# Performance work log

Hardware: AMD Instinct MI355X
Metric: run time of the kernel (lower is better)

Reference implementation:

```python
import math
import jax, jax.numpy as jnp
import numpy as np

B, T, D, V, S, R = 128, 32, 64, 4096, 32, 8
PONDER = 0.01
TWO_PI = np.float32(2.0 * math.pi)


def _ln(x, g, b, eps=1e-5):
    mu = x.mean(-1, keepdims=True)
    var = ((x - mu) ** 2).mean(-1, keepdims=True)
    return (x - mu) / jnp.sqrt(var + eps) * g + b


def _clin(xr, xi, Wr, br, Wi, bi):
    # ComplexLinear: fc_real/fc_imag share biases per torch module
    real = (xr @ Wr + br) - (xi @ Wi + bi)
    imag = (xi @ Wr + br) + (xr @ Wi + bi)
    return real, imag


def setup_inputs() -> dict:
    key = jax.random.key(0)
    ks = jax.random.split(key, 10)
    f = lambda k, sh, s: jax.random.normal(k, sh, jnp.float32) * s
    return {
        "x_seq": jax.random.randint(ks[0], (B, T), 0, V),
        "enc_emb": f(ks[1], (V, 2 * D), 0.02),
        "vq_emb": f(ks[2], (V, 2 * D), 0.05),
        "norm_rg": jnp.ones((D,), jnp.float32),
        "norm_rb": jnp.zeros((D,), jnp.float32),
        "norm_ig": jnp.ones((D,), jnp.float32),
        "norm_ib": jnp.zeros((D,), jnp.float32),
        "proj_w": f(ks[3], (3, 2, D, D), 0.05),  # [q/k/v, real/imag, in, out]
        "proj_b": f(ks[4], (3, 2, D), 0.01),
        "mem_gate_w": f(ks[5], (2 * D, 1), 0.05),
        "mem_gate_b": jnp.zeros((1,), jnp.float32),
        "arb_w": f(ks[6], (2 * D, 3), 0.05),
        "arb_b": jnp.zeros((3,), jnp.float32),
        "dec_w": f(ks[7], (2 * D, V), 0.02),
        "dec_b": jnp.zeros((V,), jnp.float32),
        "halt_bias": jnp.array(3.0, jnp.float32),
        "input_gate": jnp.array(0.0, jnp.float32),
    }


def _fwd(x_seq, enc_emb, vq_emb, norm_rg, norm_rb, norm_ig, norm_ib,
         proj_w, proj_b, mem_gate_w, mem_gate_b, arb_w, arb_b,
         dec_w, dec_b, halt_bias, input_gate):
    sg = jax.lax.stop_gradient
    emb = enc_emb[x_seq]                         # [B,T,2D]
    er, ei = emb[..., :D], emb[..., D:]
    alpha = jax.nn.sigmoid(input_gate)
    bias = jax.nn.softplus(halt_bias)
    vq_sq = (vq_emb ** 2).sum(-1)                # [V]

    def step(carry, xs):
        gw_r, gw_i, mem_r, mem_i = carry
        x_r, x_i = xs
        gw_r = alpha * gw_r + (1.0 - alpha) * x_r
        gw_i = alpha * gw_i + (1.0 - alpha) * x_i
        active = jnp.ones((x_r.shape[0],), jnp.float32)
        acc_vq = jnp.zeros_like(active)
        acc_ppx = jnp.zeros_like(active)
        acc_ent = jnp.zeros_like(active)
        acc_pond = jnp.zeros_like(active)
        acc_ph = jnp.zeros_like(active)
        prev_ang = jnp.arctan2(gw_i, gw_r)
        for _ in range(R):
            cr = _ln(gw_r, norm_rg, norm_rb)
            ci = _ln(gw_i, norm_ig, norm_ib)
            flat = jnp.concatenate([cr, ci], -1)            # [B,2D]
            # VQ (argmin over squared euclidean == argmin over cdist)
            d2 = (flat ** 2).sum(-1, keepdims=True) - 2.0 * (flat @ vq_emb.T) + vq_sq
            idx = jnp.argmin(d2, -1)                        # [B]
            zq = vq_emb[idx]                                # [B,2D]
            vq_loss = ((zq - sg(flat)) ** 2).mean(-1) + 0.25 * ((sg(zq) - flat) ** 2).mean(-1)
            zq_st = flat + sg(zq - flat)                    # straight-through
            avg = jax.nn.one_hot(idx, V, dtype=jnp.float32).mean(0)
            ent = -(avg * jnp.log(avg + 1e-10)).sum()
            ppx = jnp.exp(ent)
            vq_r, vq_i = zq_st[:, :D], zq_st[:, D:]
            # Hermitian gating
            qr, qi = _clin(cr, ci, proj_w[0, 0], proj_b[0, 0], proj_w[0, 1], proj_b[0, 1])
            kr, ki = _clin(cr, ci, proj_w[1, 0], proj_b[1, 0], proj_w[1, 1], proj_b[1, 1])
            wr, wi = _clin(cr, ci, proj_w[2, 0], proj_b[2, 0], proj_w[2, 1], proj_b[2, 1])
            gate = jax.nn.sigmoid((qr * kr + qi * ki).sum(-1, keepdims=True))
            g_r, g_i = wr * gate, wi * gate
            # memory read (mem unchanged during recursion)
            sim = jnp.einsum('bsd,bd->bs', mem_r, cr) + jnp.einsum('bsd,bd->bs', mem_i, ci)
            attn = jax.nn.softmax(sim, -1)
            m_r = jnp.einsum('bs,bsd->bd', attn, mem_r)
            m_i = jnp.einsum('bs,bsd->bd', attn, mem_i)
            # arbitrator mix
            gates = jax.nn.softmax(flat @ arb_w + arb_b, -1)  # [B,3]
            u_r = gates[:, 0:1] * g_r + gates[:, 1:2] * m_r + gates[:, 2:3] * vq_r
            u_i = gates[:, 0:1] * g_i + gates[:, 1:2] * m_i + gates[:, 2:3] * vq_i
            c_r = 0.6 * cr + 0.4 * u_r
            c_i = 0.6 * ci + 0.4 * u_i
            ang = jnp.arctan2(c_i, c_r)
            diff = jnp.abs(ang - prev_ang)
            diff = jnp.minimum(diff, TWO_PI - diff)
            acc_ph = acc_ph + active * diff.mean(-1)
            prev_ang = ang
            halt = jax.nn.sigmoid(bias - vq_loss)
            stop = (halt > 0.5).astype(jnp.float32)
            acc_pond = acc_pond + active * PONDER
            m = active > 0.5
            acc_vq = jnp.where(m, vq_loss, acc_vq)
            acc_ppx = jnp.where(m, ppx, acc_ppx)
            acc_ent = jnp.where(m, ent, acc_ent)
            gw_r = jnp.where(m[:, None], c_r, gw_r)
            gw_i = jnp.where(m[:, None], c_i, gw_i)
            active = active * (1.0 - stop)
        # final memory write (read output discarded, matching torch)
        flat_gw = jnp.concatenate([gw_r, gw_i], -1)
        wg = jax.nn.sigmoid(flat_gw @ mem_gate_w + mem_gate_b)  # [B,1]
        sh_r = jnp.roll(mem_r, 1, axis=1)
        sh_i = jnp.roll(mem_i, 1, axis=1)
        mem_r = sh_r.at[:, 0].set(wg * gw_r + (1.0 - wg) * sh_r[:, 0])
        mem_i = sh_i.at[:, 0].set(wg * gw_i + (1.0 - wg) * sh_i[:, 0])
        stats = jnp.stack([acc_vq.mean(), acc_ppx.mean(), acc_ent.mean(),
                           acc_pond.mean(), acc_ph.mean()])
        return (gw_r, gw_i, mem_r, mem_i), (gw_r, gw_i, stats)

    init = (jnp.zeros((B, D), jnp.float32), jnp.zeros((B, D), jnp.float32),
            jnp.zeros((B, S, D), jnp.float32), jnp.zeros((B, S, D), jnp.float32))
    xs = (jnp.moveaxis(er, 1, 0), jnp.moveaxis(ei, 1, 0))
    (gw_r, gw_i, mem_r, mem_i), (o_r, o_i, stats) = jax.lax.scan(step, init, xs)
    flat_out = jnp.concatenate([jnp.moveaxis(o_r, 0, 1), jnp.moveaxis(o_i, 0, 1)], -1)  # [B,T,2D]
    logits = flat_out @ dec_w + dec_b
    return logits, stats.mean(0), mem_r, mem_i


def reference(x_seq, enc_emb, vq_emb, norm_rg, norm_rb, norm_ig, norm_ib,
              proj_w, proj_b, mem_gate_w, mem_gate_b, arb_w, arb_b,
              dec_w, dec_b, halt_bias, input_gate):
    return _fwd(x_seq, enc_emb, vq_emb, norm_rg, norm_rb, norm_ig, norm_ib,
                proj_w, proj_b, mem_gate_w, mem_gate_b, arb_w, arb_b,
                dec_w, dec_b, halt_bias, input_gate)
```

## Files before the change

### kernel.cpp

```cpp
#include <hip/hip_runtime.h>
#include <math.h>

#define BB 128
#define TT 32
#define DDIM 64
#define VV 4096
#define SS 32
#define RR 8
#define NT 512
#define SMP 65

typedef unsigned short u16;
typedef unsigned int u32;
typedef _Float16 h2 __attribute__((ext_vector_type(2)));

__device__ __forceinline__ h2 bch(u32 u){ union { u32 u; h2 h; } v; v.u = u; return v.h; }

__device__ __forceinline__ float fdot2f(u32 a, u32 b, float acc){
#if __has_builtin(__builtin_amdgcn_fdot2)
  return __builtin_amdgcn_fdot2(bch(a), bch(b), acc, false);
#else
  h2 x = bch(a), y = bch(b);
  return acc + (float)x[0] * (float)y[0] + (float)x[1] * (float)y[1];
#endif
}

__device__ __forceinline__ u32 packh2(float a, float b){
  union { _Float16 h[2]; u32 u; } p;
  p.h[0] = (_Float16)a; p.h[1] = (_Float16)b;
  return p.u;
}

__device__ __forceinline__ void bar(){ __syncthreads(); }

__global__ __launch_bounds__(256) void k_pack(const float* __restrict__ vq, u32* __restrict__ vqT){
  int gid = blockIdx.x * 256 + threadIdx.x;
  int l   = gid & 63;
  int dc8 = (gid >> 6) & 15;
  int c0  = gid >> 10;
  int c   = (c0 << 6) + l;
  const float4* s4 = (const float4*)(vq + c * 128 + dc8 * 8);
  float4 lo = s4[0], hi = s4[1];
  uint4 o;
  o.x = packh2(lo.x, lo.y);
  o.y = packh2(lo.z, lo.w);
  o.z = packh2(hi.x, hi.y);
  o.w = packh2(hi.z, hi.w);
  ((uint4*)vqT)[gid] = o;
}

__global__ __launch_bounds__(256) void k_vqsq(const float* __restrict__ vq, float* __restrict__ vqsq){
  int c = blockIdx.x * 256 + threadIdx.x;
  const float4* v4 = (const float4*)(vq + c * 128);
  float s = 0.f;
  #pragma unroll
  for (int d = 0; d < 32; d++){
    float4 v = v4[d];
    s = fmaf(v.x, v.x, s); s = fmaf(v.y, v.y, s);
    s = fmaf(v.z, v.z, s); s = fmaf(v.w, v.w, s);
  }
  vqsq[c] = s;
}

__global__ __launch_bounds__(NT) void k_recur(
    const int* __restrict__ x_seq, const float* __restrict__ enc_emb,
    const float* __restrict__ vq_emb, const u32* __restrict__ vqT,
    const float* __restrict__ vq_sq,
    const float* __restrict__ nrg, const float* __restrict__ nrb,
    const float* __restrict__ nig, const float* __restrict__ nib,
    const float* __restrict__ proj_w, const float* __restrict__ proj_b,
    const float* __restrict__ mgw, const float* __restrict__ mgb,
    const float* __restrict__ arb_w, const float* __restrict__ arb_b,
    const float* __restrict__ hb, const float* __restrict__ ig,
    float* __restrict__ gwout,
    int* __restrict__ idxbuf, int* __restrict__ rstop_g, float* __restrict__ accs,
    float* __restrict__ out_mem)
{
  const int b = blockIdx.x;
  const int tid = threadIdx.x;
  const int lane = tid & 63;
  const int wave = tid >> 6;

  __shared__ __align__(16) float s_gw[128];
  __shared__ __align__(16) float s_flat[128];
  __shared__ __align__(16) u32   s_flath[64];
  __shared__ __align__(16) float s_c[128];
  __shared__ __align__(16) float s_zq[128];
  __shared__ __align__(16) float s_enext[128];
  __shared__ float s_mem[2][SS][SMP];
  __shared__ __align__(16) float s_mv[12][DDIM];
  __shared__ float s_sim[SS];
  __shared__ float s_red[8];
  __shared__ float s_cand[8];
  __shared__ int   s_candi[8];

  for (int i = tid; i < 128; i += NT) s_gw[i] = 0.f;
  for (int i = tid; i < 2 * SS * SMP; i += NT) ((float*)s_mem)[i] = 0.f;
  if (tid < 128) s_enext[tid] = enc_emb[x_seq[b * TT] * 128 + tid];
  __syncthreads();

  const float alpha = 1.f / (1.f + expf(-ig[0]));
  float bias_h; { float x = hb[0]; bias_h = log1pf(expf(x)); }
  int head = 0;
  float prev_ang = 0.f;
  float acc_ph = 0.f;

  const float pb0r = proj_b[lane],        pb0i = proj_b[64 + lane];
  const float pb1r = proj_b[128 + lane],  pb1i = proj_b[192 + lane];
  const float pb2r = proj_b[256 + lane],  pb2i = proj_b[320 + lane];

  const uint4* vqT4 = (const uint4*)vqT;

  #pragma unroll 1
  for (int t = 0; t < TT; t++){
    if (tid < 128){
      s_gw[tid] = alpha * s_gw[tid] + (1.f - alpha) * s_enext[tid];
    }
    bar();
    if (wave == 2) prev_ang = atan2f(s_gw[64 + lane], s_gw[lane]);

    float vl_last = 0.f;
    if (wave == 2) acc_ph = 0.f;
    int rst = 0;
    bool stop = false;

    #pragma unroll 1
    for (int r = 0; r < RR; r++){
      if (wave < 2){
        float x = s_gw[wave * 64 + lane];
        float mu = x;
        #pragma unroll
        for (int m = 1; m < 64; m <<= 1) mu += __shfl_xor(mu, m);
        mu *= (1.f / 64.f);
        float dxl = x - mu;
        float vv = dxl * dxl;
        #pragma unroll
        for (int m = 1; m < 64; m <<= 1) vv += __shfl_xor(vv, m);
        vv *= (1.f / 64.f);
        float rs = 1.f / sqrtf(vv + 1e-5f);
        const float* g  = wave ? nig : nrg;
        const float* bb = wave ? nib : nrb;
        float fv = dxl * rs * g[lane] + bb[lane];
        s_flat[wave * 64 + lane] = fv;
        float pv = __shfl_xor(fv, 1);
        if ((lane & 1) == 0)
          s_flath[(wave * 64 + lane) >> 1] = packh2(fv, pv);
      }
      bar();

      uint4 F[16];
      {
        const uint4* sfh4 = (const uint4*)s_flath;
        #pragma unroll
        for (int i = 0; i < 16; i++) F[i] = sfh4[i];
      }
      float bsc = 3.4e38f; int bidx = 0;
      #pragma unroll 1
      for (int k = 0; k < 8; k++){
        int c0 = wave + 8 * k;
        int c  = (c0 << 6) + lane;
        float qv = vq_sq[c];
        const uint4* vp = vqT4 + (c0 * 16) * 64 + lane;
        uint4 U[16];
        #pragma unroll
        for (int dc8 = 0; dc8 < 16; dc8++) U[dc8] = vp[dc8 * 64];
        float a0 = 0.f, a1 = 0.f, a2 = 0.f, a3 = 0.f;
        #pragma unroll
        for (int dc8 = 0; dc8 < 16; dc8 += 4){
          a0 = fdot2f(U[dc8+0].x, F[dc8+0].x, a0); a0 = fdot2f(U[dc8+0].y, F[dc8+0].y, a0);
          a0 = fdot2f(U[dc8+0].z, F[dc8+0].z, a0); a0 = fdot2f(U[dc8+0].w, F[dc8+0].w, a0);
          a1 = fdot2f(U[dc8+1].x, F[dc8+1].x, a1); a1 = fdot2f(U[dc8+1].y, F[dc8+1].y, a1);
          a1 = fdot2f(U[dc8+1].z, F[dc8+1].z, a1); a1 = fdot2f(U[dc8+1].w, F[dc8+1].w, a1);
          a2 = fdot2f(U[dc8+2].x, F[dc8+2].x, a2); a2 = fdot2f(U[dc8+2].y, F[dc8+2].y, a2);
          a2 = fdot2f(U[dc8+2].z, F[dc8+2].z, a2); a2 = fdot2f(U[dc8+2].w, F[dc8+2].w, a2);
          a3 = fdot2f(U[dc8+3].x, F[dc8+3].x, a3); a3 = fdot2f(U[dc8+3].y, F[dc8+3].y, a3);
          a3 = fdot2f(U[dc8+3].z, F[dc8+3].z, a3); a3 = fdot2f(U[dc8+3].w, F[dc8+3].w, a3);
        }
        float dot = (a0 + a1) + (a2 + a3);
        float sc = qv - 2.f * dot;
        if (sc < bsc || (sc == bsc && c < bidx)){ bsc = sc; bidx = c; }
      }
      #pragma unroll
      for (int m = 1; m < 64; m <<= 1){
        float os = __shfl_xor(bsc, m);
        int   oi = __shfl_xor(bidx, m);
        if (os < bsc || (os == bsc && oi < bidx)){ bsc = os; bidx = oi; }
      }
      if (lane == 0){ s_cand[wave] = bsc; s_candi[wave] = bidx; }
      bar();

      if (wave >= 2){
        if (wave == 3 && r == 0 && t + 1 < TT){
          int xn = x_seq[b * TT + t + 1];
          s_enext[lane]      = enc_emb[xn * 128 + lane];
          s_enext[64 + lane] = enc_emb[xn * 128 + 64 + lane];
        }
        const int w2 = wave - 2;
        const int p = w2 >> 1, wsel = w2 & 1;
        const float* W = proj_w + ((p * 2 + wsel) << 12);
        float a0=0.f,a1=0.f,a2=0.f,a3=0.f;
        float b0=0.f,b1=0.f,b2=0.f,b3=0.f;
        #pragma unroll
        for (int i = 0; i < 64; i += 4){
          float4 xr4 = *(const float4*)&s_flat[i];
          float4 xi4 = *(const float4*)&s_flat[64 + i];
          float w0 = W[(i + 0) * 64 + lane];
          float w1 = W[(i + 1) * 64 + lane];
          float w2v= W[(i + 2) * 64 + lane];
          float w3 = W[(i + 3) * 64 + lane];
          a0 = fmaf(xr4.x, w0, a0); a1 = fmaf(xr4.y, w1, a1);
          a2 = fmaf(xr4.z, w2v, a2); a3 = fmaf(xr4.w, w3, a3);
          b0 = fmaf(xi4.x, w0, b0); b1 = fmaf(xi4.y, w1, b1);
          b2 = fmaf(xi4.z, w2v, b2); b3 = fmaf(xi4.w, w3, b3);
        }
        s_mv[w2 * 2 + 0][lane] = (a0 + a1) + (a2 + a3);
        s_mv[w2 * 2 + 1][lane] = (b0 + b1) + (b2 + b3);
      } else if (wave == 0){
        const int s2 = lane & 31, h = lane >> 5;
        const float* mrow = &s_mem[h][s2][0];
        const float* fx = s_flat + h * 64;
        float a0=0.f,a1=0.f,a2=0.f,a3=0.f;
        #pragma unroll
        for (int d = 0; d < 64; d += 4){
          a0 = fmaf(mrow[d + 0], fx[d + 0], a0);
          a1 = fmaf(mrow[d + 1], fx[d + 1], a1);
          a2 = fmaf(mrow[d + 2], fx[d + 2], a2);
          a3 = fmaf(mrow[d + 3], fx[d + 3], a3);
        }
        float p = (a0 + a1) + (a2 + a3);
        p += __shfl_xor(p, 32);
        float mx = p;
        #pragma unroll
        for (int m = 1; m < 32; m <<= 1) mx = fmaxf(mx, __shfl_xor(mx, m));
        float e = expf(p - mx);
        float sm = e;
        #pragma unroll
        for (int m = 1; m < 32; m <<= 1) sm += __shfl_xor(sm, m);
        if (lane < 32) s_sim[lane] = e / sm;
      } else {
        float bs = s_cand[0]; int bi = s_candi[0];
        #pragma unroll
        for (int w = 1; w < 8; w++){
          float os = s_cand[w]; int oi = s_candi[w];
          if (os < bs || (os == bs && oi < bi)){ bs = os; bi = oi; }
        }
        int imin = __builtin_amdgcn_readfirstlane(bi);
        float f0 = s_flat[lane], f1 = s_flat[64 + lane];
        float p0 = fmaf(f0, arb_w[lane * 3 + 0], f1 * arb_w[(64 + lane) * 3 + 0]);
        float p1 = fmaf(f0, arb_w[lane * 3 + 1], f1 * arb_w[(64 + lane) * 3 + 1]);
        float p2 = fmaf(f0, arb_w[lane * 3 + 2], f1 * arb_w[(64 + lane) * 3 + 2]);
        float z0 = vq_emb[imin * 128 + lane];
        float z1 = vq_emb[imin * 128 + 64 + lane];
        s_zq[lane]      = z0;
        s_zq[64 + lane] = z1;
        float d0 = z0 - f0, d1 = z1 - f1;
        float sq = d0 * d0 + d1 * d1;
        #pragma unroll
        for (int m = 1; m < 64; m <<= 1){
          p0 += __shfl_xor(p0, m); p1 += __shfl_xor(p1, m);
          p2 += __shfl_xor(p2, m); sq += __shfl_xor(sq, m);
        }
        if (lane == 0){
          s_red[4] = p0 + arb_b[0];
          s_red[5] = p1 + arb_b[1];
          s_red[6] = p2 + arb_b[2];
          s_red[0] = 1.25f * sq * (1.f / 128.f);
          idxbuf[(b * TT + t) * RR + r] = imin;
        }
      }
      bar();

      float vl = s_red[0];
      stop = (bias_h - vl) > 0.f;
      vl_last = vl; rst = r;

      if (tid < 128){
        float qr = s_mv[0][lane] - s_mv[3][lane] + pb0r - pb0i;
        float qi = s_mv[1][lane] + s_mv[2][lane] + pb0r + pb0i;
        float kr = s_mv[4][lane] - s_mv[7][lane] + pb1r - pb1i;
        float ki = s_mv[5][lane] + s_mv[6][lane] + pb1r + pb1i;
        float g = fmaf(qr, kr, qi * ki);
        #pragma unroll
        for (int m = 1; m < 64; m <<= 1) g += __shfl_xor(g, m);
        float gate = 1.f / (1.f + expf(-g));
        const int h = wave, j = lane;
        float m_reg = 0.f;
        #pragma unroll 8
        for (int s2 = 0; s2 < 32; s2++)
          m_reg = fmaf(s_sim[s2], s_mem[h][s2][j], m_reg);
        float l0 = s_red[4], l1 = s_red[5], l2 = s_red[6];
        float mx = fmaxf(l0, fmaxf(l1, l2));
        float e0 = expf(l0 - mx), e1 = expf(l1 - mx), e2 = expf(l2 - mx);
        float inv = 1.f / (e0 + e1 + e2);
        float zq = s_zq[tid];
        float wv = h ? (s_mv[9][j] + s_mv[10][j] + pb2r + pb2i)
                     : (s_mv[8][j] - s_mv[11][j] + pb2r - pb2i);
        float u = (e0 * inv) * (gate * wv) + (e1 * inv) * m_reg + (e2 * inv) * zq;
        float cv = 0.6f * s_flat[tid] + 0.4f * u;
        s_c[tid]  = cv;
        s_gw[tid] = cv;
      }
      bar();

      if (wave == 2){
        float ang = atan2f(s_c[64 + lane], s_c[lane]);
        float df = fabsf(ang - prev_ang);
        df = fminf(df, 6.28318530717958647692f - df);
        prev_ang = ang;
        #pragma unroll
        for (int m = 1; m < 64; m <<= 1) df += __shfl_xor(df, m);
        acc_ph += df * (1.f / 64.f);
        if ((stop || r == RR - 1) && lane == 0)
          accs[(b * TT + t) * 4 + 2] = acc_ph;
      }
      if (stop) break;
    }

    float pond = 0.01f * (float)(rst + 1);
    if (tid < 128) gwout[(b * TT + t) * 128 + tid] = s_gw[tid];
    head = (head + SS - 1) & (SS - 1);
    if (wave < 2){
      float p = fmaf(s_c[lane], mgw[lane], s_c[64 + lane] * mgw[64 + lane]);
      #pragma unroll
      for (int m = 1; m < 64; m <<= 1) p += __shfl_xor(p, m);
      float wg = 1.f / (1.f + expf(-(p + mgb[0])));
      const int h = wave, d0 = lane;
      float old = s_mem[h][head][d0];
      s_mem[h][head][d0] = wg * s_c[h * 64 + d0] + (1.f - wg) * old;
    }
    if (tid == 0){
      int o = b * TT + t;
      rstop_g[o] = rst;
      accs[o * 4 + 0] = vl_last;
      accs[o * 4 + 1] = pond;
    }
  }

  bar();
  for (int i = tid; i < SS * DDIM; i += NT){
    int s2 = i >> 6, d0 = i & 63;
    int ph = (head + s2) & (SS - 1);
    out_mem[b * SS * DDIM + i] = s_mem[0][ph][d0];
    out_mem[BB * SS * DDIM + b * SS * DDIM + i] = s_mem[1][ph][d0];
  }
}

__global__ __launch_bounds__(256) void k_max(const int* __restrict__ rstop_g,
                                             int* __restrict__ maxr,
                                             float* __restrict__ out_stats){
  __shared__ int sm[8][TT];
  int tid = threadIdx.x;
  int t = tid & 31, q = tid >> 5;
  int mx = 0;
  for (int b = q * 16; b < q * 16 + 16; b++) mx = max(mx, rstop_g[b * TT + t]);
  sm[q][t] = mx;
  __syncthreads();
  if (tid < TT){
    int m = sm[0][tid];
    #pragma unroll
    for (int qq = 1; qq < 8; qq++) m = max(m, sm[qq][tid]);
    maxr[tid] = m;
  } else if (tid >= 64 && tid < 69){
    out_stats[tid - 64] = 0.f;
  }
}

__global__ __launch_bounds__(256) void k_tail(
    const u32* __restrict__ vqT, const float* __restrict__ vq_sq,
    const float* __restrict__ gwout, const int* __restrict__ rstop_g,
    const int* __restrict__ maxr, int* __restrict__ idxbuf,
    const float* __restrict__ nrg, const float* __restrict__ nrb,
    const float* __restrict__ nig, const float* __restrict__ nib)
{
  int o = blockIdx.x;
  int t = o & (TT - 1);
  int rs = rstop_g[o];
  if (rs >= maxr[t]) return;
  __shared__ __align__(16) u32 sfh[64];
  __shared__ float s_cand[4];
  __shared__ int   s_candi[4];
  int tid = threadIdx.x, lane = tid & 63, wave = tid >> 6;
  if (wave < 2){
    float x = gwout[o * 128 + wave * 64 + lane];
    float mu = x;
    #pragma unroll
    for (int m = 1; m < 64; m <<= 1) mu += __shfl_xor(mu, m);
    mu *= (1.f / 64.f);
    float dxl = x - mu;
    float vv = dxl * dxl;
    #pragma unroll
    for (int m = 1; m < 64; m <<= 1) vv += __shfl_xor(vv, m);
    vv *= (1.f / 64.f);
    float rsn = 1.f / sqrtf(vv + 1e-5f);
    const float* g  = wave ? nig : nrg;
    const float* bb = wave ? nib : nrb;
    float fv = dxl * rsn * g[lane] + bb[lane];
    float pv = __shfl_xor(fv, 1);
    if ((lane & 1) == 0) sfh[(wave * 64 + lane) >> 1] = packh2(fv, pv);
  }
  __syncthreads();
  uint4 F[16];
  {
    const uint4* sfh4 = (const uint4*)sfh;
    #pragma unroll
    for (int i = 0; i < 16; i++) F[i] = sfh4[i];
  }
  float bsc = 3.4e38f; int bidx = 0;
  #pragma unroll 1
  for (int k = 0; k < 16; k++){
    int c0 = wave + 4 * k;
    const uint4* vp = ((const uint4*)vqT) + (c0 * 16) * 64 + lane;
    uint4 U[16];
    #pragma unroll
    for (int dc8 = 0; dc8 < 16; dc8++) U[dc8] = vp[dc8 * 64];
    float dot = 0.f;
    #pragma unroll
    for (int dc8 = 0; dc8 < 16; dc8++){
      dot = fdot2f(U[dc8].x, F[dc8].x, dot);
      dot = fdot2f(U[dc8].y, F[dc8].y, dot);
      dot = fdot2f(U[dc8].z, F[dc8].z, dot);
      dot = fdot2f(U[dc8].w, F[dc8].w, dot);
    }
    int c = c0 * 64 + lane;
    float sc = vq_sq[c] - 2.f * dot;
    if (sc < bsc || (sc == bsc && c < bidx)){ bsc = sc; bidx = c; }
  }
  #pragma unroll
  for (int m = 1; m < 64; m <<= 1){
    float os = __shfl_xor(bsc, m);
    int   oi = __shfl_xor(bidx, m);
    if (os < bsc || (os == bsc && oi < bidx)){ bsc = os; bidx = oi; }
  }
  if (lane == 0){ s_cand[wave] = bsc; s_candi[wave] = bidx; }
  __syncthreads();
  if (tid == 0){
    float bs = s_cand[0]; int bi = s_candi[0];
    for (int w = 1; w < 4; w++){
      float os = s_cand[w]; int oi = s_candi[w];
      if (os < bs || (os == bs && oi < bi)){ bs = os; bi = oi; }
    }
    for (int r = rs + 1; r < RR; r++) idxbuf[o * RR + r] = bi;
  }
}

__global__ __launch_bounds__(512) void k_stats(
    const int* __restrict__ idxbuf, const int* __restrict__ rstop_g,
    const float* __restrict__ accs, const int* __restrict__ maxr,
    float* __restrict__ out_stats)
{
  __shared__ int   s_vals[8][128];
  __shared__ float s_ent2[RR];
  __shared__ float s_part[8][5];
  const int t = blockIdx.x;
  int tid = threadIdx.x, lane = tid & 63, wave = tid >> 6;
  int mr = maxr[t];
  int r = wave;
  if (r <= mr){
    int v1 = idxbuf[(lane * TT + t) * RR + r];
    int v2 = idxbuf[((64 + lane) * TT + t) * RR + r];
    s_vals[wave][lane]      = v1;
    s_vals[wave][64 + lane] = v2;
    int c1 = 0, c2 = 0;
    for (int j = 0; j < 128; j++){
      int v = s_vals[wave][j];
      c1 += (v == v1); c2 += (v == v2);
    }
    float contrib = -(logf((float)c1 * (1.f / 128.f) + 1e-10f)
                    + logf((float)c2 * (1.f / 128.f) + 1e-10f)) * (1.f / 128.f);
    #pragma unroll
    for (int m = 1; m < 64; m <<= 1) contrib += __shfl_xor(contrib, m);
    if (lane == 0) s_ent2[r] = contrib;
  }
  __syncthreads();

  float sv = 0.f, sp = 0.f, se = 0.f, sn = 0.f, sh = 0.f;
  if (tid < BB){
    int o = tid * TT + t;
    int rs = rstop_g[o];
    float ent = s_ent2[rs];
    se = ent;
    sp = expf(ent);
    sv = accs[o * 4 + 0];
    sn = accs[o * 4 + 1];
    sh = accs[o * 4 + 2];
  }
  #pragma unroll
  for (int m = 1; m < 64; m <<= 1){
    sv += __shfl_xor(sv, m); sp += __shfl_xor(sp, m); se += __shfl_xor(se, m);
    sn += __shfl_xor(sn, m); sh += __shfl_xor(sh, m);
  }
  if (lane == 0){
    s_part[wave][0] = sv; s_part[wave][1] = sp; s_part[wave][2] = se;
    s_part[wave][3] = sn; s_part[wave][4] = sh;
  }
  __syncthreads();
  if (tid == 0){
    float a[5] = {0.f, 0.f, 0.f, 0.f, 0.f};
    for (int w = 0; w < 8; w++)
      for (int j = 0; j < 5; j++) a[j] += s_part[w][j];
    const float inv = 1.f / (float)(BB * TT);
    for (int j = 0; j < 5; j++) atomicAdd(&out_stats[j], a[j] * inv);
  }
}

__global__ __launch_bounds__(256) void k_dec(
    const float* __restrict__ gwout, const float* __restrict__ dec_w,
    const float* __restrict__ dec_b, float* __restrict__ out)
{
  __shared__ float At[32][128];
  int tid = threadIdx.x;
  int row0 = blockIdx.y * 32;
  int col0 = blockIdx.x * 256;
  {
    const float4* src = (const float4*)(gwout + row0 * 128);
    float4* dst = (float4*)&At[0][0];
    for (int i = tid; i < 1024; i += 256) dst[i] = src[i];
  }
  __syncthreads();
  int v = col0 + tid;
  float acc[32];
  #pragma unroll
  for (int r2 = 0; r2 < 32; r2++) acc[r2] = 0.f;
  for (int k = 0; k < 128; k += 4){
    float w0 = dec_w[(k + 0) * 4096 + v];
    float w1 = dec_w[(k + 1) * 4096 + v];
    float w2 = dec_w[(k + 2) * 4096 + v];
    float w3 = dec_w[(k + 3) * 4096 + v];
    #pragma unroll
    for (int r2 = 0; r2 < 32; r2++){
      float4 a = *(const float4*)&At[r2][k];
      acc[r2] = fmaf(a.x, w0, fmaf(a.y, w1, fmaf(a.z, w2, fmaf(a.w, w3, acc[r2]))));
    }
  }
  float bv = dec_b[v];
  for (int r2 = 0; r2 < 32; r2++)
    out[(row0 + r2) * 4096 + v] = acc[r2] + bv;
}

extern "C" void kernel_launch(void* const* d_in, const int* in_sizes, int n_in,
                              void* d_out, int out_size, void* d_ws, size_t ws_size,
                              hipStream_t stream){
  const int*   x_seq   = (const int*)  d_in[0];
  const float* enc_emb = (const float*)d_in[1];
  const float* vq_emb  = (const float*)d_in[2];
  const float* nrg     = (const float*)d_in[3];
  const float* nrb     = (const float*)d_in[4];
  const float* nig     = (const float*)d_in[5];
  const float* nib     = (const float*)d_in[6];
  const float* proj_w  = (const float*)d_in[7];
  const float* proj_b  = (const float*)d_in[8];
  const float* mgw     = (const float*)d_in[9];
  const float* mgb     = (const float*)d_in[10];
  const float* arb_w   = (const float*)d_in[11];
  const float* arb_b   = (const float*)d_in[12];
  const float* dec_w   = (const float*)d_in[13];
  const float* dec_b   = (const float*)d_in[14];
  const float* hb      = (const float*)d_in[15];
  const float* ig      = (const float*)d_in[16];

  char* ws = (char*)d_ws;
  u32*   vqT    = (u32*)  (ws + 0);
  float* vqsq   = (float*)(ws + 2097152);
  float* gwout  = (float*)(ws + 2113536);
  int*   idxbuf = (int*)  (ws + 6307840);
  int*   rstop  = (int*)  (ws + 6438912);
  float* accs   = (float*)(ws + 6455296);
  int*   maxr   = (int*)  (ws + 6520832);

  float* out = (float*)d_out;
  float* out_stats = out + 16777216;
  float* out_mem   = out + 16777221;

  k_pack <<<dim3(256), dim3(256), 0, stream>>>(vq_emb, vqT);
  k_vqsq <<<dim3(16),  dim3(256), 0, stream>>>(vq_emb, vqsq);
  k_recur<<<dim3(BB),  dim3(NT),  0, stream>>>(
      x_seq, enc_emb, vq_emb, vqT, vqsq,
      nrg, nrb, nig, nib, proj_w, proj_b, mgw, mgb, arb_w, arb_b, hb, ig,
      gwout, idxbuf, rstop, accs, out_mem);
  k_dec  <<<dim3(16, 128), dim3(256), 0, stream>>>(gwout, dec_w, dec_b, out);
  k_max  <<<dim3(1),   dim3(256), 0, stream>>>(rstop, maxr, out_stats);
  k_tail <<<dim3(BB * TT), dim3(256), 0, stream>>>(vqT, vqsq, gwout, rstop, maxr, idxbuf,
                                                   nrg, nrb, nig, nib);
  k_stats<<<dim3(TT),  dim3(512), 0, stream>>>(idxbuf, rstop, accs, maxr, out_stats);
}
```

Before: 636.4 us.

## Double-buffer VQ codebook streaming through LDS via async global_load_lds

The nearest-codebook search now stages each wave's fp16 codebook slices into a per-wave double buffer in LDS using global_load_lds, with explicit vmcnt waits so the next chunk loads while the current one is dotted. The vq_sq norms are also prefetched into registers before the loop. The aim is to hide global memory latency inside the serial per-step search and to cut register pressure from the 16 uint4 loads. In exchange it adds 128 KB of LDS per block, which may limit occupancy or exceed the LDS budget, and it relies on hand-written waitcnt ordering being correct.

```diff
diff --git a/kernel.cpp b/kernel.cpp
--- a/kernel.cpp
+++ b/kernel.cpp
@@ -9,6 +9,12 @@
 #define RR 8
 #define NT 512
 #define SMP 65
+
+#if defined(__has_builtin)
+#if __has_builtin(__builtin_amdgcn_global_load_lds)
+#define HAS_GLLDS 1
+#endif
+#endif
 
 typedef unsigned short u16;
 typedef unsigned int u32;
@@ -60,6 +66,38 @@
     s = fmaf(v.z, v.z, s); s = fmaf(v.w, v.w, s);
   }
   vqsq[c] = s;
+}
+
+#if HAS_GLLDS
+__device__ __forceinline__ void stage8(const uint4* gsrc, uint4* lds){
+  #pragma unroll
+  for (int j = 0; j < 8; j++)
+    __builtin_amdgcn_global_load_lds(
+        (const __attribute__((address_space(1))) void*)(gsrc + j * 64),
+        (__attribute__((address_space(3))) void*)(lds + j * 64),
+        16, 0, 0);
+}
+#endif
+
+__device__ __forceinline__ void dotLds(const uint4* buf, const uint4 (&F)[16], int off, int lane,
+                                       float& a0, float& a1, float& a2, float& a3){
+  #pragma unroll
+  for (int j = 0; j < 8; j += 4){
+    uint4 u0 = buf[(j + 0) * 64 + lane];
+    uint4 u1 = buf[(j + 1) * 64 + lane];
+    uint4 u2 = buf[(j + 2) * 64 + lane];
+    uint4 u3 = buf[(j + 3) * 64 + lane];
+    uint4 f0 = F[off + j + 0], f1 = F[off + j + 1];
+    uint4 f2 = F[off + j + 2], f3 = F[off + j + 3];
+    a0 = fdot2f(u0.x, f0.x, a0); a0 = fdot2f(u0.y, f0.y, a0);
+    a0 = fdot2f(u0.z, f0.z, a0); a0 = fdot2f(u0.w, f0.w, a0);
+    a1 = fdot2f(u1.x, f1.x, a1); a1 = fdot2f(u1.y, f1.y, a1);
+    a1 = fdot2f(u1.z, f1.z, a1); a1 = fdot2f(u1.w, f1.w, a1);
+    a2 = fdot2f(u2.x, f2.x, a2); a2 = fdot2f(u2.y, f2.y, a2);
+    a2 = fdot2f(u2.z, f2.z, a2); a2 = fdot2f(u2.w, f2.w, a2);
+    a3 = fdot2f(u3.x, f3.x, a3); a3 = fdot2f(u3.y, f3.y, a3);
+    a3 = fdot2f(u3.z, f3.z, a3); a3 = fdot2f(u3.w, f3.w, a3);
+  }
 }
 
 __global__ __launch_bounds__(NT) void k_recur(
@@ -93,6 +131,9 @@
   __shared__ float s_red[8];
   __shared__ float s_cand[8];
   __shared__ int   s_candi[8];
+#if HAS_GLLDS
+  __shared__ __align__(16) uint4 s_vstg[8][2][8][64];
+#endif
 
   for (int i = tid; i < 128; i += NT) s_gw[i] = 0.f;
   for (int i = tid; i < 2 * SS * SMP; i += NT) ((float*)s_mem)[i] = 0.f;
@@ -148,45 +189,65 @@
       }
       bar();
 
-      uint4 F[16];
       {
-        const uint4* sfh4 = (const uint4*)s_flath;
-        #pragma unroll
-        for (int i = 0; i < 16; i++) F[i] = sfh4[i];
+        uint4 F[16];
+        {
+          const uint4* sfh4 = (const uint4*)s_flath;
+          #pragma unroll
+          for (int i = 0; i < 16; i++) F[i] = sfh4[i];
+        }
+        float Q[8];
+        #pragma unroll
+        for (int k = 0; k < 8; k++) Q[k] = vq_sq[((wave + 8 * k) << 6) + lane];
+
+        float bsc = 3.4e38f; int bidx = 0;
+#if HAS_GLLDS
+        uint4* stg0 = &s_vstg[wave][0][0][0];
+        uint4* stg1 = &s_vstg[wave][1][0][0];
+        const uint4* base0 = vqT4 + (wave * 16) * 64 + lane;
+        stage8(base0,          stg0);
+        stage8(base0 + 8 * 64, stg1);
+        #pragma unroll 1
+        for (int k = 0; k < 8; k++){
+          asm volatile("s_waitcnt vmcnt(8)" ::: "memory");
+          float a0 = 0.f, a1 = 0.f, a2 = 0.f, a3 = 0.f;
+          dotLds(stg0, F, 0, lane, a0, a1, a2, a3);
+          if (k < 7)
+            stage8(vqT4 + ((wave + 8 * (k + 1)) * 16) * 64 + lane, stg0);
+          if (k < 7) asm volatile("s_waitcnt vmcnt(8)" ::: "memory");
+          else       asm volatile("s_waitcnt vmcnt(0)" ::: "memory");
+          dotLds(stg1, F, 8, lane, a0, a1, a2, a3);
+          if (k < 7)
+            stage8(vqT4 + ((wave + 8 * (k + 1)) * 16 + 8) * 64 + lane, stg1);
+          float dot = (a0 + a1) + (a2 + a3);
+          int c = ((wave + 8 * k) << 6) + lane;
+          float sc = Q[k] - 2.f * dot;
+          if (sc < bsc || (sc == bsc && c < bidx)){ bsc = sc; bidx = c; }
+        }
+#else
+        #pragma unroll 1
+        for (int k = 0; k < 8; k++){
+          int c = ((wave + 8 * k) << 6) + lane;
+          const uint4* vp = vqT4 + ((wave + 8 * k) * 16) * 64 + lane;
+          uint4 U[16];
+          #pragma unroll
+          for (int dc8 = 0; dc8 < 16; dc8++) U[dc8] = vp[dc8 * 64];
+          float a0 = 0.f, a1 = 0.f, a2 = 0.f, a3 = 0.f;
+          dotLds(U, F, 0, 0, a0, a1, a2, a3);
+          dotLds(U + 8, F, 8, 0, a0, a1, a2, a3);
+          float dot = (a0 + a1) + (a2 + a3);
+          float sc = Q[k] - 2.f * dot;
+          if (sc < bsc || (sc == bsc && c < bidx)){ bsc = sc; bidx = c; }
+        }
+#endif
+        #pragma unroll
+        for (int m = 1; m < 64; m <<= 1){
+          float os = __shfl_xor(bsc, m);
+          int   oi = __shfl_xor(bidx, m);
+          if (os < bsc || (os == bsc && oi < bidx)){ bsc = os; bidx = oi; }
+        }
+        if (lane == 0){ s_cand[wave] = bsc; s_candi[wave] = bidx; }
       }
-      float bsc = 3.4e38f; int bidx = 0;
-      #pragma unroll 1
-      for (int k = 0; k < 8; k++){
-        int c0 = wave + 8 * k;
-        int c  = (c0 << 6) + lane;
-        float qv = vq_sq[c];
-        const uint4* vp = vqT4 + (c0 * 16) * 64 + lane;
-        uint4 U[16];
-        #pragma unroll
-        for (int dc8 = 0; dc8 < 16; dc8++) U[dc8] = vp[dc8 * 64];
-        float a0 = 0.f, a1 = 0.f, a2 = 0.f, a3 = 0.f;
-        #pragma unroll
-        for (int dc8 = 0; dc8 < 16; dc8 += 4){
-          a0 = fdot2f(U[dc8+0].x, F[dc8+0].x, a0); a0 = fdot2f(U[dc8+0].y, F[dc8+0].y, a0);
-          a0 = fdot2f(U[dc8+0].z, F[dc8+0].z, a0); a0 = fdot2f(U[dc8+0].w, F[dc8+0].w, a0);
-          a1 = fdot2f(U[dc8+1].x, F[dc8+1].x, a1); a1 = fdot2f(U[dc8+1].y, F[dc8+1].y, a1);
-          a1 = fdot2f(U[dc8+1].z, F[dc8+1].z, a1); a1 = fdot2f(U[dc8+1].w, F[dc8+1].w, a1);
-          a2 = fdot2f(U[dc8+2].x, F[dc8+2].x, a2); a2 = fdot2f(U[dc8+2].y, F[dc8+2].y, a2);
-          a2 = fdot2f(U[dc8+2].z, F[dc8+2].z, a2); a2 = fdot2f(U[dc8+2].w, F[dc8+2].w, a2);
-          a3 = fdot2f(U[dc8+3].x, F[dc8+3].x, a3); a3 = fdot2f(U[dc8+3].y, F[dc8+3].y, a3);
-          a3 = fdot2f(U[dc8+3].z, F[dc8+3].z, a3); a3 = fdot2f(U[dc8+3].w, F[dc8+3].w, a3);
-        }
-        float dot = (a0 + a1) + (a2 + a3);
-        float sc = qv - 2.f * dot;
-        if (sc < bsc || (sc == bsc && c < bidx)){ bsc = sc; bidx = c; }
-      }
-      #pragma unroll
-      for (int m = 1; m < 64; m <<= 1){
-        float os = __shfl_xor(bsc, m);
-        int   oi = __shfl_xor(bidx, m);
-        if (os < bsc || (os == bsc && oi < bidx)){ bsc = os; bidx = oi; }
-      }
-      if (lane == 0){ s_cand[wave] = bsc; s_candi[wave] = bidx; }
       bar();
 
       if (wave >= 2){
```

Result: slower. 767.4 us (+20.6%).
